# Kernel tuning notes

Hardware: AMD Instinct MI355X
Metric: run time of the kernel (lower is better)

## Reference

```python
import jax, jax.numpy as jnp
import numpy as np

IN_CH = 8        # input_channels (includes time channel)
HID = 64         # hidden_channels
OUT = 1          # output_channels
MLP_W = 128      # CDEFunc hidden width
B, T = 4096, 166


def setup_inputs() -> dict:
    key = jax.random.key(0)
    ks = jax.random.split(key, 12)
    s = lambda fan_in: 1.0 / np.sqrt(fan_in)
    u0 = jax.random.normal(ks[0], (B, IN_CH - 1), dtype=jnp.float32)
    coeffs = jax.random.normal(ks[1], (B, T, IN_CH), dtype=jnp.float32)
    # CDEFunc params
    W1 = jax.random.uniform(ks[2], (HID, MLP_W), jnp.float32, -s(HID), s(HID))
    b1 = jax.random.uniform(ks[3], (MLP_W,), jnp.float32, -s(HID), s(HID))
    W2 = jax.random.uniform(ks[4], (MLP_W, IN_CH * HID), jnp.float32, -s(MLP_W), s(MLP_W))
    b2 = jax.random.uniform(ks[5], (IN_CH * HID,), jnp.float32, -s(MLP_W), s(MLP_W))
    # initial / readout linears
    Wi = jax.random.uniform(ks[6], (IN_CH - 1, HID), jnp.float32, -s(IN_CH - 1), s(IN_CH - 1))
    bi = jax.random.uniform(ks[7], (HID,), jnp.float32, -s(IN_CH - 1), s(IN_CH - 1))
    Wr = jax.random.uniform(ks[8], (HID, OUT), jnp.float32, -s(HID), s(HID))
    br = jax.random.uniform(ks[9], (OUT,), jnp.float32, -s(HID), s(HID))
    return {"u0": u0, "coeffs": coeffs, "W1": W1, "b1": b1, "W2": W2,
            "b2": b2, "Wi": Wi, "bi": bi, "Wr": Wr, "br": br}


def _cde_forward(u0, coeffs, W1, b1, W2, b2, Wi, bi, Wr, br):
    z0 = u0 @ Wi + bi                                  # [B, HID]
    # Linear interpolation on the knot grid t=0..T-1 with Euler steps of dt=1:
    # z_{k+1} = z_k + f(z_k) @ (X_{k+1} - X_k)
    dX = coeffs[:, 1:] - coeffs[:, :-1]                # [B, T-1, IN_CH]
    dX_t = jnp.swapaxes(dX, 0, 1)                      # [T-1, B, IN_CH]

    def step(z, dx):
        h = jax.nn.relu(z @ W1 + b1)                   # [B, MLP_W]
        f = jnp.tanh(h @ W2 + b2)                      # [B, IN_CH*HID]
        f = f.reshape(z.shape[0], HID, IN_CH)          # [B, HID, IN_CH]
        z_new = z + jnp.einsum('bhi,bi->bh', f, dx)
        return z_new, z_new

    _, zs = jax.lax.scan(step, z0, dX_t)               # [T-1, B, HID]
    z_all = jnp.concatenate([z0[None], zs], axis=0)    # [T, B, HID]
    z_all = jnp.swapaxes(z_all, 0, 1)                  # [B, T, HID]
    return z_all @ Wr + br                             # [B, T, OUT]


def reference(u0, coeffs, W1, b1, W2, b2, Wi, bi, Wr, br):
    return _cde_forward(u0, coeffs, W1, b1, W2, b2, Wi, bi, Wr, br)
```

## Files before the change

kernel.cpp:

```cpp
#include <hip/hip_runtime.h>


#define NBLK 256
#define NT   512
#define RB   16
#define T_LEN 166
#define NSTEP 165
#define IC   8
#define HID  64
#define MW   128
#define NF   512

typedef _Float16 half8 __attribute__((ext_vector_type(8)));
typedef _Float16 half4 __attribute__((ext_vector_type(4)));
typedef float    f32x4 __attribute__((ext_vector_type(4)));

__device__ __forceinline__ float fast_tanh(float x) {
    float e = __expf(2.0f * x);
    return 1.0f - 2.0f * __builtin_amdgcn_rcpf(e + 1.0f);
}

__device__ __forceinline__ void bar_lgkm() {
    asm volatile("s_waitcnt lgkmcnt(0)" ::: "memory");
    __builtin_amdgcn_s_barrier();
    __builtin_amdgcn_sched_barrier(0);
}

__global__ __launch_bounds__(NT, 2)
void cde_fused(const float* __restrict__ u0, const float* __restrict__ coeffs,
               const float* __restrict__ W1, const float* __restrict__ b1,
               const float* __restrict__ W2, const float* __restrict__ b2,
               const float* __restrict__ Wi, const float* __restrict__ bi,
               const float* __restrict__ Wr, const float* __restrict__ br,
               float* __restrict__ out)
{
    __shared__ __align__(16) unsigned char hh[RB * 256];
    __shared__ __align__(16) unsigned char hl[RB * 256];
    __shared__ __align__(16) unsigned char zh[RB * 128];
    __shared__ __align__(16) unsigned char zl[RB * 128];
    __shared__ float part[8][17];

    const int tid  = threadIdx.x;
    const int lane = tid & 63;
    const int w    = tid >> 6;
    const int l15  = lane & 15;
    const int lq   = lane >> 4;
    const int swzr = (l15 & 7) << 4;
    const int b0   = blockIdx.x * RB;

    half8 w1h[2], w1l[2];
    #pragma unroll
    for (int kt = 0; kt < 2; ++kt) {
        const int krow = kt * 32 + lq * 8;
        const int ncol = w * 16 + l15;
        half8 vh, vl;
        #pragma unroll
        for (int j = 0; j < 8; ++j) {
            const float x = W1[(krow + j) * MW + ncol];
            const _Float16 hi = (_Float16)x;
            vh[j] = hi; vl[j] = (_Float16)(x - (float)hi);
        }
        w1h[kt] = vh; w1l[kt] = vl;
    }
    half8 w2h[16], w2l[16];
    #pragma unroll
    for (int q = 0; q < 4; ++q) {
        #pragma unroll
        for (int kt = 0; kt < 4; ++kt) {
            const int krow = kt * 32 + lq * 8;
            const int ncol = (w * 4 + q) * 16 + l15;
            half8 vh, vl;
            #pragma unroll
            for (int j = 0; j < 8; ++j) {
                const float x = W2[(krow + j) * NF + ncol];
                const _Float16 hi = (_Float16)x;
                vh[j] = hi; vl[j] = (_Float16)(x - (float)hi);
            }
            w2h[q * 4 + kt] = vh; w2l[q * 4 + kt] = vl;
        }
    }
    const f32x4 b1v = *(const f32x4*)(b1 + w * 16 + lq * 4);
    f32x4 b2v[4];
    #pragma unroll
    for (int q = 0; q < 4; ++q)
        b2v[q] = *(const f32x4*)(b2 + (w * 4 + q) * 16 + lq * 4);

    float wrs[8];
    #pragma unroll
    for (int j = 0; j < 8; ++j) wrs[j] = Wr[w * 8 + j];
    const float brv = br[0];

    float z8[8];
    {
        float uu[7];
        const float* ur = u0 + (size_t)(b0 + l15) * 7;
        #pragma unroll
        for (int c = 0; c < 7; ++c) uu[c] = ur[c];
        #pragma unroll
        for (int j = 0; j < 8; ++j) {
            float a = bi[w * 8 + j];
            #pragma unroll
            for (int c = 0; c < 7; ++c) a = fmaf(uu[c], Wi[c * HID + w * 8 + j], a);
            z8[j] = a;
        }
    }
    {
        half8 hi8, lo8;
        #pragma unroll
        for (int j = 0; j < 8; ++j) {
            const _Float16 hi = (_Float16)z8[j];
            hi8[j] = hi; lo8[j] = (_Float16)(z8[j] - (float)hi);
        }
        if (lq == 0) {
            const int zoff = l15 * 128 + ((w * 16) ^ swzr);
            *(half8*)(zh + zoff) = hi8;
            *(half8*)(zl + zoff) = lo8;
            float rp = 0.f;
            #pragma unroll
            for (int j = 0; j < 8; ++j) rp = fmaf(z8[j], wrs[j], rp);
            part[w][l15] = rp;
        }
    }
    const float* cbase = coeffs + (size_t)(b0 + l15) * T_LEN * IC + (lq & 1) * 4;
    f32x4 ccur = *(const f32x4*)(cbase);
    __syncthreads();

    for (int t = 0; t < NSTEP; ++t) {
        const f32x4 cnext = *(const f32x4*)(cbase + (size_t)(t + 1) * IC);

        if (w == 7) {
            float v = part[lq][l15] + part[lq + 4][l15];
            v += __shfl_xor(v, 16, 64);
            v += __shfl_xor(v, 32, 64);
            if (lq == 0) out[(size_t)(b0 + l15) * T_LEN + t] = v + brv;
        }

        f32x4 acc1 = {0.f, 0.f, 0.f, 0.f};
        #pragma unroll
        for (int kt = 0; kt < 2; ++kt) {
            const int off = l15 * 128 + ((kt * 64 + lq * 16) ^ swzr);
            const half8 zfh = *(const half8*)(zh + off);
            const half8 zfl = *(const half8*)(zl + off);
            acc1 = __builtin_amdgcn_mfma_f32_16x16x32_f16(w1h[kt], zfh, acc1, 0, 0, 0);
            acc1 = __builtin_amdgcn_mfma_f32_16x16x32_f16(w1l[kt], zfh, acc1, 0, 0, 0);
            acc1 = __builtin_amdgcn_mfma_f32_16x16x32_f16(w1h[kt], zfl, acc1, 0, 0, 0);
        }
        half4 ph, pl;
        #pragma unroll
        for (int r = 0; r < 4; ++r) {
            const float hv = fmaxf(acc1[r] + b1v[r], 0.0f);
            const _Float16 hi = (_Float16)hv;
            ph[r] = hi; pl[r] = (_Float16)(hv - (float)hi);
        }
        const int hoff = l15 * 256 + ((w * 32 + lq * 8) ^ swzr);
        *(half4*)(hh + hoff) = ph;
        *(half4*)(hl + hoff) = pl;
        bar_lgkm();

        half8 bhf[4], blf[4];
        #pragma unroll
        for (int kt = 0; kt < 4; ++kt) {
            const int off = l15 * 256 + ((kt * 64 + lq * 16) ^ swzr);
            bhf[kt] = *(const half8*)(hh + off);
            blf[kt] = *(const half8*)(hl + off);
        }
        const f32x4 dxv = cnext - ccur;
        #pragma unroll
        for (int q = 0; q < 4; ++q) {
            f32x4 acc = {0.f, 0.f, 0.f, 0.f};
            #pragma unroll
            for (int kt = 0; kt < 4; ++kt) {
                acc = __builtin_amdgcn_mfma_f32_16x16x32_f16(w2h[q * 4 + kt], bhf[kt], acc, 0, 0, 0);
                acc = __builtin_amdgcn_mfma_f32_16x16x32_f16(w2l[q * 4 + kt], bhf[kt], acc, 0, 0, 0);
                acc = __builtin_amdgcn_mfma_f32_16x16x32_f16(w2h[q * 4 + kt], blf[kt], acc, 0, 0, 0);
            }
            float s = 0.f;
            #pragma unroll
            for (int r = 0; r < 4; ++r)
                s = fmaf(fast_tanh(acc[r] + b2v[q][r]), dxv[r], s);
            const float tt = s + __shfl_xor(s, 16, 64);
            const float uu = __shfl_xor(tt, 32, 64);
            z8[2 * q]     += tt;
            z8[2 * q + 1] += uu;
        }
        {
            half8 hi8, lo8;
            #pragma unroll
            for (int j = 0; j < 8; ++j) {
                const _Float16 hi = (_Float16)z8[j];
                hi8[j] = hi; lo8[j] = (_Float16)(z8[j] - (float)hi);
            }
            if (lq == 0) {
                const int zoff = l15 * 128 + ((w * 16) ^ swzr);
                *(half8*)(zh + zoff) = hi8;
                *(half8*)(zl + zoff) = lo8;
                float rp = 0.f;
                #pragma unroll
                for (int j = 0; j < 8; ++j) rp = fmaf(z8[j], wrs[j], rp);
                part[w][l15] = rp;
            }
        }
        ccur = cnext;
        bar_lgkm();
    }

    if (w == 7) {
        float v = part[lq][l15] + part[lq + 4][l15];
        v += __shfl_xor(v, 16, 64);
        v += __shfl_xor(v, 32, 64);
        if (lq == 0) out[(size_t)(b0 + l15) * T_LEN + NSTEP] = v + brv;
    }
}

extern "C" void kernel_launch(void* const* d_in, const int* in_sizes, int n_in,
                              void* d_out, int out_size, void* d_ws, size_t ws_size,
                              hipStream_t stream) {
    const float* u0     = (const float*)d_in[0];
    const float* coeffs = (const float*)d_in[1];
    const float* W1     = (const float*)d_in[2];
    const float* b1     = (const float*)d_in[3];
    const float* W2     = (const float*)d_in[4];
    const float* b2     = (const float*)d_in[5];
    const float* Wi     = (const float*)d_in[6];
    const float* bi     = (const float*)d_in[7];
    const float* Wr     = (const float*)d_in[8];
    const float* br     = (const float*)d_in[9];
    cde_fused<<<NBLK, NT, 0, stream>>>(u0, coeffs, W1, b1, W2, b2, Wi, bi, Wr, br,
                                       (float*)d_out);
}
```

Measured before the change: 305.6 us.

## Split MFMA accumulators, use permlane swaps for reductions, and fold biases

The W1 and W2 MFMA products are reorganised into two independent accumulator sets per output tile, issued kt-outer and q-inner, so consecutive MFMAs no longer wait on each other. Biases are folded into the accumulator initial values, and the cross-lane shuffles are replaced by v_permlane16/32_swap sums. The z hi/lo stores and the readout partial are emitted per half as soon as those values are ready, and the sched_barrier is removed so the compiler can schedule more freely. The aim is to cut latency in the serial per-step chain, at the cost of more accumulator registers and inline assembly.

```diff
diff --git a/kernel.cpp b/kernel.cpp
--- a/kernel.cpp
+++ b/kernel.cpp
@@ -23,7 +23,19 @@
 __device__ __forceinline__ void bar_lgkm() {
     asm volatile("s_waitcnt lgkmcnt(0)" ::: "memory");
     __builtin_amdgcn_s_barrier();
-    __builtin_amdgcn_sched_barrier(0);
+}
+
+__device__ __forceinline__ float sum_xor16(float x) {
+    float a = x, b;
+    asm("v_mov_b32 %0, %1" : "=v"(b) : "v"(x));
+    asm("v_permlane16_swap_b32 %0, %1" : "+v"(a), "+v"(b));
+    return a + b;
+}
+__device__ __forceinline__ float sum_xor32(float x) {
+    float a = x, b;
+    asm("v_mov_b32 %0, %1" : "=v"(b) : "v"(x));
+    asm("v_permlane32_swap_b32 %0, %1" : "+v"(a), "+v"(b));
+    return a + b;
 }
 
 __global__ __launch_bounds__(NT, 2)
@@ -45,6 +57,7 @@
     const int w    = tid >> 6;
     const int l15  = lane & 15;
     const int lq   = lane >> 4;
+    const bool hi32 = (lane & 32) != 0;
     const int swzr = (l15 & 7) << 4;
     const int b0   = blockIdx.x * RB;
 
@@ -106,18 +119,17 @@
     }
     {
         half8 hi8, lo8;
+        float rp = 0.f;
         #pragma unroll
         for (int j = 0; j < 8; ++j) {
             const _Float16 hi = (_Float16)z8[j];
             hi8[j] = hi; lo8[j] = (_Float16)(z8[j] - (float)hi);
+            rp = fmaf(z8[j], wrs[j], rp);
         }
         if (lq == 0) {
             const int zoff = l15 * 128 + ((w * 16) ^ swzr);
             *(half8*)(zh + zoff) = hi8;
             *(half8*)(zl + zoff) = lo8;
-            float rp = 0.f;
-            #pragma unroll
-            for (int j = 0; j < 8; ++j) rp = fmaf(z8[j], wrs[j], rp);
             part[w][l15] = rp;
         }
     }
@@ -130,25 +142,28 @@
 
         if (w == 7) {
             float v = part[lq][l15] + part[lq + 4][l15];
-            v += __shfl_xor(v, 16, 64);
-            v += __shfl_xor(v, 32, 64);
+            v = sum_xor32(sum_xor16(v));
             if (lq == 0) out[(size_t)(b0 + l15) * T_LEN + t] = v + brv;
         }
 
-        f32x4 acc1 = {0.f, 0.f, 0.f, 0.f};
-        #pragma unroll
-        for (int kt = 0; kt < 2; ++kt) {
-            const int off = l15 * 128 + ((kt * 64 + lq * 16) ^ swzr);
-            const half8 zfh = *(const half8*)(zh + off);
-            const half8 zfl = *(const half8*)(zl + off);
-            acc1 = __builtin_amdgcn_mfma_f32_16x16x32_f16(w1h[kt], zfh, acc1, 0, 0, 0);
-            acc1 = __builtin_amdgcn_mfma_f32_16x16x32_f16(w1l[kt], zfh, acc1, 0, 0, 0);
-            acc1 = __builtin_amdgcn_mfma_f32_16x16x32_f16(w1h[kt], zfl, acc1, 0, 0, 0);
-        }
+        const int zo0 = l15 * 128 + ((lq * 16) ^ swzr);
+        const int zo1 = l15 * 128 + ((64 + lq * 16) ^ swzr);
+        const half8 zfh0 = *(const half8*)(zh + zo0);
+        const half8 zfl0 = *(const half8*)(zl + zo0);
+        const half8 zfh1 = *(const half8*)(zh + zo1);
+        const half8 zfl1 = *(const half8*)(zl + zo1);
+        f32x4 a1A = b1v;
+        f32x4 a1B = {0.f, 0.f, 0.f, 0.f};
+        a1A = __builtin_amdgcn_mfma_f32_16x16x32_f16(w1h[0], zfh0, a1A, 0, 0, 0);
+        a1B = __builtin_amdgcn_mfma_f32_16x16x32_f16(w1h[1], zfh1, a1B, 0, 0, 0);
+        a1A = __builtin_amdgcn_mfma_f32_16x16x32_f16(w1l[0], zfh0, a1A, 0, 0, 0);
+        a1B = __builtin_amdgcn_mfma_f32_16x16x32_f16(w1l[1], zfh1, a1B, 0, 0, 0);
+        a1A = __builtin_amdgcn_mfma_f32_16x16x32_f16(w1h[0], zfl0, a1A, 0, 0, 0);
+        a1B = __builtin_amdgcn_mfma_f32_16x16x32_f16(w1h[1], zfl1, a1B, 0, 0, 0);
         half4 ph, pl;
         #pragma unroll
         for (int r = 0; r < 4; ++r) {
-            const float hv = fmaxf(acc1[r] + b1v[r], 0.0f);
+            const float hv = fmaxf(a1A[r] + a1B[r], 0.0f);
             const _Float16 hi = (_Float16)hv;
             ph[r] = hi; pl[r] = (_Float16)(hv - (float)hi);
         }
@@ -165,49 +180,65 @@
             blf[kt] = *(const half8*)(hl + off);
         }
         const f32x4 dxv = cnext - ccur;
+        f32x4 accA[4], accB[4];
         #pragma unroll
         for (int q = 0; q < 4; ++q) {
-            f32x4 acc = {0.f, 0.f, 0.f, 0.f};
-            #pragma unroll
-            for (int kt = 0; kt < 4; ++kt) {
-                acc = __builtin_amdgcn_mfma_f32_16x16x32_f16(w2h[q * 4 + kt], bhf[kt], acc, 0, 0, 0);
-                acc = __builtin_amdgcn_mfma_f32_16x16x32_f16(w2l[q * 4 + kt], bhf[kt], acc, 0, 0, 0);
-                acc = __builtin_amdgcn_mfma_f32_16x16x32_f16(w2h[q * 4 + kt], blf[kt], acc, 0, 0, 0);
-            }
+            accA[q] = b2v[q];
+            accB[q] = (f32x4){0.f, 0.f, 0.f, 0.f};
+        }
+        #pragma unroll
+        for (int kt = 0; kt < 4; ++kt) {
+            #pragma unroll
+            for (int q = 0; q < 4; ++q) {
+                accA[q] = __builtin_amdgcn_mfma_f32_16x16x32_f16(w2h[q * 4 + kt], bhf[kt], accA[q], 0, 0, 0);
+                accB[q] = __builtin_amdgcn_mfma_f32_16x16x32_f16(w2l[q * 4 + kt], bhf[kt], accB[q], 0, 0, 0);
+            }
+        }
+        #pragma unroll
+        for (int kt = 0; kt < 4; ++kt) {
+            #pragma unroll
+            for (int q = 0; q < 4; ++q) {
+                if (kt < 2) accA[q] = __builtin_amdgcn_mfma_f32_16x16x32_f16(w2h[q * 4 + kt], blf[kt], accA[q], 0, 0, 0);
+                else        accB[q] = __builtin_amdgcn_mfma_f32_16x16x32_f16(w2h[q * 4 + kt], blf[kt], accB[q], 0, 0, 0);
+            }
+        }
+        float rp = 0.f;
+        #pragma unroll
+        for (int q = 0; q < 4; ++q) {
             float s = 0.f;
             #pragma unroll
             for (int r = 0; r < 4; ++r)
-                s = fmaf(fast_tanh(acc[r] + b2v[q][r]), dxv[r], s);
-            const float tt = s + __shfl_xor(s, 16, 64);
-            const float uu = __shfl_xor(tt, 32, 64);
+                s = fmaf(fast_tanh(accA[q][r] + accB[q][r]), dxv[r], s);
+            const float tt = sum_xor16(s);
+            const float uu = sum_xor32(hi32 ? tt : 0.f);
             z8[2 * q]     += tt;
             z8[2 * q + 1] += uu;
-        }
-        {
-            half8 hi8, lo8;
-            #pragma unroll
-            for (int j = 0; j < 8; ++j) {
-                const _Float16 hi = (_Float16)z8[j];
-                hi8[j] = hi; lo8[j] = (_Float16)(z8[j] - (float)hi);
-            }
-            if (lq == 0) {
-                const int zoff = l15 * 128 + ((w * 16) ^ swzr);
-                *(half8*)(zh + zoff) = hi8;
-                *(half8*)(zl + zoff) = lo8;
-                float rp = 0.f;
+            rp = fmaf(z8[2 * q], wrs[2 * q], rp);
+            rp = fmaf(z8[2 * q + 1], wrs[2 * q + 1], rp);
+            if (q & 1) {
+                const int c0 = 4 * (q >> 1);
+                half4 h4, l4;
                 #pragma unroll
-                for (int j = 0; j < 8; ++j) rp = fmaf(z8[j], wrs[j], rp);
-                part[w][l15] = rp;
-            }
-        }
+                for (int j = 0; j < 4; ++j) {
+                    const float zv = z8[c0 + j];
+                    const _Float16 hi = (_Float16)zv;
+                    h4[j] = hi; l4[j] = (_Float16)(zv - (float)hi);
+                }
+                if (lq == 0) {
+                    const int zoff = l15 * 128 + ((w * 16) ^ swzr) + c0 * 2;
+                    *(half4*)(zh + zoff) = h4;
+                    *(half4*)(zl + zoff) = l4;
+                }
+            }
+        }
+        if (lq == 0) part[w][l15] = rp;
         ccur = cnext;
         bar_lgkm();
     }
 
     if (w == 7) {
         float v = part[lq][l15] + part[lq + 4][l15];
-        v += __shfl_xor(v, 16, 64);
-        v += __shfl_xor(v, 32, 64);
+        v = sum_xor32(sum_xor16(v));
         if (lq == 0) out[(size_t)(b0 + l15) * T_LEN + NSTEP] = v + brv;
     }
 }
```

Result: slower. 395.5 us (+29.4%).
